# Kernel tuning notes

Hardware: AMD Instinct MI355X
Metric: run time of the kernel (lower is better)

The kernel has to match this reference:

```python
import jax, jax.numpy as jnp
import numpy as np

L = 3          # encoder layers
H, D = 12, 64  # heads, head_dim
DM = H * D     # 768
DF = 3072
WH = WW = 14
S = WH * WW + 1            # 197 tokens incl. cls
ND = (2*WH-1)*(2*WW-1) + 3  # 732 rel-pos entries
EPS = 1e-12


def _make_rel_idx():
    coords = np.stack(np.meshgrid(np.arange(WH), np.arange(WW), indexing='ij'))
    coords = coords.reshape(2, -1)                      # [2, 196]
    rel = (coords[:, :, None] - coords[:, None, :]).transpose(1, 2, 0)  # [196,196,2]
    rel[:, :, 0] += WH - 1
    rel[:, :, 1] += WW - 1
    rel[:, :, 0] *= 2 * WW - 1
    idx = np.zeros((S, S), dtype=np.int32)
    idx[1:, 1:] = rel.sum(-1)
    idx[0, :] = ND - 3
    idx[:, 0] = ND - 2
    idx[0, 0] = ND - 1
    return jnp.asarray(idx.flatten())

REL_IDX = _make_rel_idx()


def _ln(x, g, b):
    m = jnp.mean(x, -1, keepdims=True)
    v = jnp.mean(jnp.square(x - m), -1, keepdims=True)
    return (x - m) * jax.lax.rsqrt(v + EPS) * g + b


def setup_inputs() -> dict:
    key = jax.random.key(0)
    ks = iter(jax.random.split(key, 32))
    p = lambda *s: jax.random.normal(next(ks), s, jnp.float32) * 0.02
    inp = {
        'x': jax.random.normal(next(ks), (64, WH, WW, DM), jnp.float32),
        'cls': p(1, 1, DM),
        'g1': jnp.ones((L, DM)), 'b1': jnp.zeros((L, DM)),
        'Wq': p(L, DM, DM), 'bq': jnp.zeros((L, DM)),
        'Wk': p(L, DM, DM),
        'Wv': p(L, DM, DM), 'bv': jnp.zeros((L, DM)),
        'rel_tbl': p(L, ND, H),
        'Wo': p(L, DM, DM), 'bo': jnp.zeros((L, DM)),
        'lam1': jnp.full((L, DM), 0.1),
        'g2': jnp.ones((L, DM)), 'b2': jnp.zeros((L, DM)),
        'Wi': p(L, DM, DF), 'bi': jnp.zeros((L, DF)),
        'Wmo': p(L, DF, DM), 'bmo': jnp.zeros((L, DM)),
        'lam2': jnp.full((L, DM), 0.1),
    }
    return inp


def reference(x, cls, g1, b1, Wq, bq, Wk, Wv, bv, rel_tbl, Wo, bo, lam1,
              g2, b2, Wi, bi, Wmo, bmo, lam2):
    B = x.shape[0]
    # patchemb: NHWC -> NCHW -> [B, C, HW] -> [B, HW, C], prepend cls token
    t = jnp.transpose(x, (0, 3, 1, 2)).reshape(B, DM, WH * WW)
    t = jnp.transpose(t, (0, 2, 1))
    h = jnp.concatenate([jnp.broadcast_to(cls, (B, 1, DM)), t], axis=1)  # [B,S,DM]

    scale = 1.0 / np.sqrt(D)
    for i in range(L):
        r = h
        hn = _ln(h, g1[i], b1[i])
        q = (hn @ Wq[i] + bq[i]).reshape(B, S, H, D)
        k = (hn @ Wk[i]).reshape(B, S, H, D)
        v = (hn @ Wv[i] + bv[i]).reshape(B, S, H, D)
        scores = jnp.einsum('bqhd,bkhd->bhqk', q, k) * scale   # [B,H,S,S]
        rel = rel_tbl[i][REL_IDX].reshape(S, S, H)             # gather bias table
        scores = scores + jnp.transpose(rel, (2, 0, 1))[None]
        probs = jax.nn.softmax(scores, axis=-1)
        ctx = jnp.einsum('bhqk,bkhd->bqhd', probs, v).reshape(B, S, DM)
        h = r + (ctx @ Wo[i] + bo[i]) * lam1[i]
        r = h
        hn = _ln(h, g2[i], b2[i])
        ff = jax.nn.gelu(hn @ Wi[i] + bi[i], approximate=False) @ Wmo[i] + bmo[i]
        h = r + ff * lam2[i]
    return h  # final encoder output [B, S, DM]
```

## Files before the change

### kernel.cpp

```cpp
#include <hip/hip_runtime.h>

#define DMM 768
#define DFF 3072
#define NH  12
#define HD  64
#define SQ  197
#define BA  64
#define NDD 732
#define MROWS (BA*SQ)
#define MPAD  12672
#define PCOLS 224
#define KS2   72
#define VTS   232
#define QS    2304
#define BIASN (NH*208*208)

typedef unsigned short u16;
typedef __bf16 bf16x8 __attribute__((ext_vector_type(8)));
typedef float  f32x4  __attribute__((ext_vector_type(4)));
typedef unsigned short us8 __attribute__((ext_vector_type(8)));

__device__ __forceinline__ float b2f(u16 u) {
    unsigned v = ((unsigned)u) << 16;
    float f; __builtin_memcpy(&f, &v, 4); return f;
}
__device__ __forceinline__ u16 f2b(float f) {
    unsigned v; __builtin_memcpy(&v, &f, 4);
    unsigned r = v + 0x7FFFu + ((v >> 16) & 1u);
    return (u16)(r >> 16);
}
__device__ __forceinline__ float gelu_exact(float x) {
    return 0.5f * x * (1.0f + erff(x * 0.70710678118654752f));
}
__device__ __forceinline__ void gload16(const u16* g, u16* l) {
    __builtin_amdgcn_global_load_lds(
        (const __attribute__((address_space(1))) unsigned int*)(g),
        (__attribute__((address_space(3))) unsigned int*)(l), 16, 0, 0);
}
__device__ __forceinline__ void hard_barrier() {
    asm volatile("s_waitcnt lgkmcnt(0)" ::: "memory");
    __builtin_amdgcn_s_barrier();
}

__global__ void patch_k(const float* __restrict__ x, const float* __restrict__ cls,
                        float* __restrict__ h) {
    long idx = (long)blockIdx.x * 256 + threadIdx.x;
    if (idx >= (long)MPAD * DMM) return;
    long r = idx / DMM; int c = (int)(idx % DMM);
    float v = 0.0f;
    if (r < MROWS) {
        int b = (int)(r / SQ), s = (int)(r % SQ);
        v = (s == 0) ? cls[c] : x[((long)b * 196 + (s - 1)) * DMM + c];
    }
    h[idx] = v;
}

__global__ void out_k(const float* __restrict__ h, float* __restrict__ out) {
    long idx = (long)blockIdx.x * 256 + threadIdx.x;
    if (idx < (long)MROWS * DMM) out[idx] = h[idx];
}

__global__ __launch_bounds__(256) void tcast_k(const float* __restrict__ in,
                                               u16* __restrict__ out,
                                               int Kd, int Nd) {
    __shared__ float t[32][33];
    int k0 = blockIdx.x * 32, n0 = blockIdx.y * 32;
    int tx = threadIdx.x & 31, ty = threadIdx.x >> 5;
    #pragma unroll
    for (int i = 0; i < 4; ++i)
        t[tx][ty + 8 * i] = in[(long)(k0 + ty + 8 * i) * Nd + n0 + tx];
    __syncthreads();
    #pragma unroll
    for (int i = 0; i < 4; ++i)
        out[(long)(n0 + ty + 8 * i) * Kd + k0 + tx] = f2b(t[ty + 8 * i][tx]);
}

__global__ __launch_bounds__(256) void tcast4_k(
    const float* __restrict__ s0, const float* __restrict__ s1,
    const float* __restrict__ s2, const float* __restrict__ s3,
    u16* __restrict__ d0, u16* __restrict__ d1,
    u16* __restrict__ d2, u16* __restrict__ d3) {
    __shared__ float t[32][33];
    int z = blockIdx.z;
    const float* in = (z == 0) ? s0 : (z == 1) ? s1 : (z == 2) ? s2 : s3;
    u16* out = (z == 0) ? d0 : (z == 1) ? d1 : (z == 2) ? d2 : d3;
    int k0 = blockIdx.x * 32, n0 = blockIdx.y * 32;
    int tx = threadIdx.x & 31, ty = threadIdx.x >> 5;
    #pragma unroll
    for (int i = 0; i < 4; ++i)
        t[tx][ty + 8 * i] = in[(long)(k0 + ty + 8 * i) * DMM + n0 + tx];
    __syncthreads();
    #pragma unroll
    for (int i = 0; i < 4; ++i)
        out[(long)(n0 + ty + 8 * i) * DMM + k0 + tx] = f2b(t[ty + 8 * i][tx]);
}

__global__ __launch_bounds__(256) void ln_k(const float* __restrict__ h,
                                            const float* __restrict__ g,
                                            const float* __restrict__ b,
                                            u16* __restrict__ hn) {
    int row = blockIdx.x, tid = threadIdx.x;
    const float* hr = h + (long)row * DMM;
    float x0 = hr[tid], x1 = hr[tid + 256], x2 = hr[tid + 512];
    float s = x0 + x1 + x2, sq = x0 * x0 + x1 * x1 + x2 * x2;
    #pragma unroll
    for (int m = 32; m > 0; m >>= 1) {
        s  += __shfl_xor(s,  m, 64);
        sq += __shfl_xor(sq, m, 64);
    }
    __shared__ float ls[4], lq[4];
    int w = tid >> 6;
    if ((tid & 63) == 0) { ls[w] = s; lq[w] = sq; }
    __syncthreads();
    s  = ls[0] + ls[1] + ls[2] + ls[3];
    sq = lq[0] + lq[1] + lq[2] + lq[3];
    float mean = s * (1.0f / DMM);
    float var  = fmaxf(sq * (1.0f / DMM) - mean * mean, 0.0f);
    float rs = rsqrtf(var + 1e-12f);
    u16* hnr = hn + (long)row * DMM;
    hnr[tid]       = f2b((x0 - mean) * rs * g[tid]       + b[tid]);
    hnr[tid + 256] = f2b((x1 - mean) * rs * g[tid + 256] + b[tid + 256]);
    hnr[tid + 512] = f2b((x2 - mean) * rs * g[tid + 512] + b[tid + 512]);
}

template <int EPI>
__global__ __launch_bounds__(256) void gemm_bt(
    const u16* __restrict__ A, const u16* __restrict__ BT,
    const float* __restrict__ bias, u16* __restrict__ outB,
    float* __restrict__ hio, const float* __restrict__ lam,
    int K, int N) {
    __shared__ __align__(16) u16 pool[24576];
    int tid = threadIdx.x;
    int w = tid >> 6, lane = tid & 63;
    int wr = w >> 1, wc = w & 1;
    int m16 = lane & 15;
    int kq  = (lane >> 4) * 8;
    int kq4 = (lane >> 4) * 4;

    int nwg = gridDim.x, bid = blockIdx.x;
    int qd = nwg >> 3, rm = nwg & 7;
    int xcd = bid & 7, seq = bid >> 3;
    int wg = (xcd < rm ? xcd * (qd + 1) : rm * (qd + 1) + (xcd - rm) * qd) + seq;
    int ntn = N >> 7;
    long m0 = (long)(wg / ntn) * 128;
    long n0 = (long)(wg % ntn) * 128;

    f32x4 acc[4][4] = {};

    int row_a = tid >> 2;
    int col_a = (tid & 3) * 8;
    const u16* gA0 = &A[(m0 + row_a) * (long)K + col_a];
    const u16* gA1 = &A[(m0 + 64 + row_a) * (long)K + col_a];
    const u16* gB0 = &BT[(n0 + row_a) * (long)K + col_a];
    const u16* gB1 = &BT[(n0 + 64 + row_a) * (long)K + col_a];
    int wo = w * 512;

    u16* const b0 = pool;
    u16* const b1 = pool + 8192;
    u16* const b2 = pool + 16384;

    auto stage = [&](int k, u16* buf) {
        int k0 = k << 5;
        gload16(gA0 + k0, buf + wo);
        gload16(gA1 + k0, buf + 2048 + wo);
        gload16(gB0 + k0, buf + 4096 + wo);
        gload16(gB1 + k0, buf + 6144 + wo);
    };
    auto compute = [&](const u16* buf) {
        bf16x8 af[4], bf[4];
        #pragma unroll
        for (int i = 0; i < 4; ++i)
            af[i] = *(const bf16x8*)&buf[(wr * 64 + i * 16 + m16) * 32 + kq];
        #pragma unroll
        for (int j = 0; j < 4; ++j)
            bf[j] = *(const bf16x8*)&buf[4096 + (wc * 64 + j * 16 + m16) * 32 + kq];
        __builtin_amdgcn_s_setprio(1);
        #pragma unroll
        for (int i = 0; i < 4; ++i)
            #pragma unroll
            for (int j = 0; j < 4; ++j)
                acc[i][j] = __builtin_amdgcn_mfma_f32_16x16x32_bf16(
                    af[i], bf[j], acc[i][j], 0, 0, 0);
        __builtin_amdgcn_s_setprio(0);
    };

    const int nsteps = K >> 5;
    stage(0, b0);
    stage(1, b1);
    const int niter = nsteps / 3 - 1;
    for (int it = 0; it < niter; ++it) {
        int k = it * 3;
        asm volatile("s_waitcnt vmcnt(4)" ::: "memory");
        __builtin_amdgcn_s_barrier();
        stage(k + 2, b2);
        compute(b0);
        asm volatile("s_waitcnt vmcnt(4)" ::: "memory");
        __builtin_amdgcn_s_barrier();
        stage(k + 3, b0);
        compute(b1);
        asm volatile("s_waitcnt vmcnt(4)" ::: "memory");
        __builtin_amdgcn_s_barrier();
        stage(k + 4, b1);
        compute(b2);
    }
    asm volatile("s_waitcnt vmcnt(4)" ::: "memory");
    __builtin_amdgcn_s_barrier();
    stage(nsteps - 1, b2);
    compute(b0);
    asm volatile("s_waitcnt vmcnt(4)" ::: "memory");
    __builtin_amdgcn_s_barrier();
    compute(b1);
    asm volatile("s_waitcnt vmcnt(0)" ::: "memory");
    __builtin_amdgcn_s_barrier();
    compute(b2);

    hard_barrier();
    float* Cs = (float*)pool;
    float bcol[4];
    #pragma unroll
    for (int j = 0; j < 4; ++j)
        bcol[j] = bias ? bias[n0 + wc * 64 + j * 16 + m16] : 0.0f;
    int et4 = tid * 4;
    int colr = et4 & 127;
    f32x4 lam4 = {};
    if (EPI == 2) lam4 = *(const f32x4*)&lam[n0 + colr];

    #pragma unroll
    for (int p = 0; p < 2; ++p) {
        if (p) hard_barrier();
        if (wr == p) {
            #pragma unroll
            for (int i = 0; i < 4; ++i)
                #pragma unroll
                for (int j = 0; j < 4; ++j)
                    #pragma unroll
                    for (int r = 0; r < 4; ++r)
                        Cs[(i * 16 + kq4 + r) * 132 + wc * 64 + j * 16 + m16] =
                            acc[i][j][r] + bcol[j];
        }
        hard_barrier();
        #pragma unroll
        for (int k = 0; k < 8; ++k) {
            int e0 = k * 1024 + et4;
            int row = e0 >> 7;
            f32x4 v = *(const f32x4*)&Cs[row * 132 + colr];
            long gi = (m0 + p * 64 + row) * (long)N + n0 + colr;
            if (EPI == 0) {
                uint2 o;
                o.x = (unsigned)f2b(v[0]) | ((unsigned)f2b(v[1]) << 16);
                o.y = (unsigned)f2b(v[2]) | ((unsigned)f2b(v[3]) << 16);
                *(uint2*)&outB[gi] = o;
            } else if (EPI == 1) {
                uint2 o;
                o.x = (unsigned)f2b(gelu_exact(v[0])) | ((unsigned)f2b(gelu_exact(v[1])) << 16);
                o.y = (unsigned)f2b(gelu_exact(v[2])) | ((unsigned)f2b(gelu_exact(v[3])) << 16);
                *(uint2*)&outB[gi] = o;
            } else {
                f32x4 hv = *(f32x4*)&hio[gi];
                #pragma unroll
                for (int t = 0; t < 4; ++t) hv[t] += v[t] * lam4[t];
                *(f32x4*)&hio[gi] = hv;
            }
        }
    }
}

__device__ __forceinline__ int relidx(int q, int k) {
    if (q == 0 && k == 0) return NDD - 1;
    if (k == 0) return NDD - 2;
    if (q == 0) return NDD - 3;
    int a = q - 1, c = k - 1;
    int dh = a / 14 - c / 14 + 13;
    int dw = a % 14 - c % 14 + 13;
    return dh * 27 + dw;
}

__global__ void bias_k(const float* __restrict__ rel, float* __restrict__ bias,
                       const float* __restrict__ bq, const float* __restrict__ bv,
                       float* __restrict__ bqkv) {
    int idx = blockIdx.x * 256 + threadIdx.x;
    if (idx < BIASN) {
        int hh = idx / (208 * 208);
        int r = (idx / 208) % 208, c = idx % 208;
        float v = 0.0f;
        if (r < SQ && c < SQ) v = rel[relidx(r, c) * NH + hh];
        bias[idx] = v;
    } else {
        int i = idx - BIASN;
        if (i < QS)
            bqkv[i] = (i < 768) ? bq[i] : ((i < 1536) ? 0.0f : bv[i - 1536]);
    }
}

__global__ __launch_bounds__(256) void attn_qk(
    const u16* __restrict__ QKV, const float* __restrict__ bias,
    u16* __restrict__ P) {
    int bh = blockIdx.x;
    int b = bh / NH, hh = bh % NH;
    __shared__ u16 Ks[208 * KS2];
    int tid = threadIdx.x, w = tid >> 6, lane = tid & 63;
    long base = ((long)b * SQ) * QS + hh * HD;
    const u16* Qp = QKV;
    const u16* Kp = QKV + 768;
    u16* Pb = P + (long)bh * 208 * PCOLS;
    for (int idx = tid; idx < 208 * 16; idx += 256)
        Pb[(idx >> 4) * PCOLS + 208 + (idx & 15)] = 0;
    for (int idx = tid; idx < 208 * 8; idx += 256) {
        int row = idx >> 3, dg = (idx & 7) * 8;
        us8 kv = {};
        if (row < SQ) kv = *(const us8*)&Kp[base + (long)row * QS + dg];
        *(us8*)&Ks[row * KS2 + dg] = kv;
    }
    __syncthreads();
    int m16 = lane & 15, quad = lane >> 4;
    int kq8 = quad * 8, q4 = quad * 4;
    const float* bh_bias = bias + (long)hh * 208 * 208;
    for (int t = w; t < 13; t += 4) {
        int m0 = t * 16;
        int qrow = m0 + m16; if (qrow > SQ - 1) qrow = SQ - 1;
        bf16x8 a0 = *(const bf16x8*)&Qp[base + (long)qrow * QS + kq8];
        bf16x8 a1 = *(const bf16x8*)&Qp[base + (long)qrow * QS + 32 + kq8];
        f32x4 sc[13];
        #pragma unroll
        for (int n = 0; n < 13; ++n) {
            bf16x8 b0 = *(const bf16x8*)&Ks[(n * 16 + m16) * KS2 + kq8];
            bf16x8 b1 = *(const bf16x8*)&Ks[(n * 16 + m16) * KS2 + 32 + kq8];
            f32x4 z = {};
            z = __builtin_amdgcn_mfma_f32_16x16x32_bf16(a0, b0, z, 0, 0, 0);
            z = __builtin_amdgcn_mfma_f32_16x16x32_bf16(a1, b1, z, 0, 0, 0);
            sc[n] = z;
        }
        float mx[4] = {-3e38f, -3e38f, -3e38f, -3e38f};
        #pragma unroll
        for (int n = 0; n < 13; ++n) {
            int col = n * 16 + m16;
            bool valid = col < SQ;
            #pragma unroll
            for (int r = 0; r < 4; ++r) {
                float v = sc[n][r] * 0.125f + bh_bias[(m0 + q4 + r) * 208 + col];
                v = valid ? v : -3e38f;
                sc[n][r] = v;
                mx[r] = fmaxf(mx[r], v);
            }
        }
        #pragma unroll
        for (int r = 0; r < 4; ++r)
            #pragma unroll
            for (int msk = 1; msk < 16; msk <<= 1)
                mx[r] = fmaxf(mx[r], __shfl_xor(mx[r], msk, 64));
        float sum[4] = {0, 0, 0, 0};
        #pragma unroll
        for (int n = 0; n < 13; ++n)
            #pragma unroll
            for (int r = 0; r < 4; ++r) {
                float e = __expf(sc[n][r] - mx[r]);
                sc[n][r] = e;
                sum[r] += e;
            }
        #pragma unroll
        for (int r = 0; r < 4; ++r)
            #pragma unroll
            for (int msk = 1; msk < 16; msk <<= 1)
                sum[r] += __shfl_xor(sum[r], msk, 64);
        float inv[4];
        #pragma unroll
        for (int r = 0; r < 4; ++r) inv[r] = 1.0f / sum[r];
        #pragma unroll
        for (int n = 0; n < 13; ++n) {
            int col = n * 16 + m16;
            #pragma unroll
            for (int r = 0; r < 4; ++r)
                Pb[(m0 + q4 + r) * PCOLS + col] = f2b(sc[n][r] * inv[r]);
        }
    }
}

__global__ __launch_bounds__(256) void attn_pv(
    const u16* __restrict__ P, const u16* __restrict__ QKV,
    u16* __restrict__ ctx) {
    int bh = blockIdx.x;
    int b = bh / NH, hh = bh % NH;
    __shared__ u16 Vt[64 * VTS];
    int tid = threadIdx.x, w = tid >> 6, lane = tid & 63;
    long base  = ((long)b * SQ) * QS + 1536 + hh * HD;
    long basec = ((long)b * SQ) * DMM + hh * HD;
    const u16* Vp = QKV;
    for (int idx = tid; idx < 224 * 8; idx += 256) {
        int row = idx >> 3, dg = (idx & 7) * 8;
        us8 vv = {};
        if (row < SQ) vv = *(const us8*)&Vp[base + (long)row * QS + dg];
        #pragma unroll
        for (int j = 0; j < 8; ++j) Vt[(dg + j) * VTS + row] = vv[j];
    }
    __syncthreads();
    const u16* Pb = P + (long)bh * 208 * PCOLS;
    int m16 = lane & 15, quad = lane >> 4;
    int kq8 = quad * 8, q4 = quad * 4;
    for (int t = w; t < 13; t += 4) {
        int m0 = t * 16;
        f32x4 co[4] = {};
        #pragma unroll
        for (int ks = 0; ks < 7; ++ks) {
            bf16x8 ap = *(const bf16x8*)&Pb[(m0 + m16) * PCOLS + ks * 32 + kq8];
            #pragma unroll
            for (int n = 0; n < 4; ++n) {
                bf16x8 bv = *(const bf16x8*)&Vt[(n * 16 + m16) * VTS + ks * 32 + kq8];
                co[n] = __builtin_amdgcn_mfma_f32_16x16x32_bf16(ap, bv, co[n], 0, 0, 0);
            }
        }
        #pragma unroll
        for (int n = 0; n < 4; ++n) {
            int col = n * 16 + m16;
            #pragma unroll
            for (int r = 0; r < 4; ++r) {
                int qr = m0 + q4 + r;
                if (qr < SQ) ctx[basec + (long)qr * DMM + col] = f2b(co[n][r]);
            }
        }
    }
}

extern "C" void kernel_launch(void* const* d_in, const int* in_sizes, int n_in,
                              void* d_out, int out_size, void* d_ws, size_t ws_size,
                              hipStream_t stream) {
    const float* x    = (const float*)d_in[0];
    const float* cls  = (const float*)d_in[1];
    const float* g1   = (const float*)d_in[2];
    const float* b1   = (const float*)d_in[3];
    const float* Wq   = (const float*)d_in[4];
    const float* bq   = (const float*)d_in[5];
    const float* Wk   = (const float*)d_in[6];
    const float* Wv   = (const float*)d_in[7];
    const float* bv   = (const float*)d_in[8];
    const float* rel  = (const float*)d_in[9];
    const float* Wo   = (const float*)d_in[10];
    const float* bo   = (const float*)d_in[11];
    const float* lam1 = (const float*)d_in[12];
    const float* g2   = (const float*)d_in[13];
    const float* b2   = (const float*)d_in[14];
    const float* Wi   = (const float*)d_in[15];
    const float* bi   = (const float*)d_in[16];
    const float* Wmo  = (const float*)d_in[17];
    const float* bmo  = (const float*)d_in[18];
    const float* lam2 = (const float*)d_in[19];

    char* p = (char*)d_ws;
    auto alloc = [&](size_t bytes) -> void* {
        void* r = (void*)p;
        p += (bytes + 255) & ~(size_t)255;
        return r;
    };
    float* h     = (float*)alloc((size_t)MPAD * DMM * 4);
    u16*   hn    = (u16*)alloc((size_t)MPAD * DMM * 2);
    u16*   qkvb  = (u16*)alloc((size_t)MPAD * QS * 2);
    u16*   ffh   = (u16*)alloc((size_t)MPAD * DFF * 2);
    u16*   WqkvT = (u16*)alloc((size_t)QS * DMM * 2);
    u16*   WoT   = (u16*)alloc((size_t)DMM * DMM * 2);
    u16*   WiT   = (u16*)alloc((size_t)DMM * DFF * 2);
    u16*   WmoT  = (u16*)alloc((size_t)DFF * DMM * 2);
    float* biasb = (float*)alloc((size_t)NH * 208 * 208 * 4);
    float* bqkv  = (float*)alloc((size_t)QS * 4);
    u16*   ctxb  = hn;
    u16*   Pbuf  = ffh;

    patch_k<<<((long)MPAD * DMM + 255) / 256, 256, 0, stream>>>(x, cls, h);

    dim3 tg4(DMM / 32, DMM / 32, 4);
    dim3 tg2(DMM / 32, DFF / 32);
    dim3 tg3(DFF / 32, DMM / 32);
    int gqkv = (MPAD / 128) * (QS / 128);
    int g6   = (MPAD / 128) * (DMM / 128);
    int g24  = (MPAD / 128) * (DFF / 128);

    for (int i = 0; i < 3; ++i) {
        size_t wofs  = (size_t)i * DMM * DMM;
        size_t wofs2 = (size_t)i * DMM * DFF;
        tcast4_k<<<tg4, 256, 0, stream>>>(Wq + wofs, Wk + wofs, Wv + wofs, Wo + wofs,
                                          WqkvT, WqkvT + 768 * DMM,
                                          WqkvT + 2 * 768 * DMM, WoT);
        tcast_k<<<tg2, 256, 0, stream>>>(Wi + wofs2, WiT, DMM, DFF);
        tcast_k<<<tg3, 256, 0, stream>>>(Wmo + wofs2, WmoT, DFF, DMM);
        bias_k<<<(BIASN + QS + 255) / 256, 256, 0, stream>>>(
            rel + (size_t)i * NDD * NH, biasb, bq + i * DMM, bv + i * DMM, bqkv);

        ln_k<<<MPAD, 256, 0, stream>>>(h, g1 + i * DMM, b1 + i * DMM, hn);
        gemm_bt<0><<<gqkv, 256, 0, stream>>>(hn, WqkvT, bqkv, qkvb, nullptr, nullptr, DMM, QS);
        attn_qk<<<BA * NH, 256, 0, stream>>>(qkvb, biasb, Pbuf);
        attn_pv<<<BA * NH, 256, 0, stream>>>(Pbuf, qkvb, ctxb);
        gemm_bt<2><<<g6, 256, 0, stream>>>(ctxb, WoT, bo + i * DMM, nullptr, h, lam1 + i * DMM, DMM, DMM);
        ln_k<<<MPAD, 256, 0, stream>>>(h, g2 + i * DMM, b2 + i * DMM, hn);
        gemm_bt<1><<<g24, 256, 0, stream>>>(hn, WiT, bi + i * DFF, ffh, nullptr, nullptr, DMM, DFF);
        gemm_bt<2><<<g6, 256, 0, stream>>>(ffh, WmoT, bmo + i * DMM, nullptr, h, lam2 + i * DMM, DFF, DMM);
    }

    out_k<<<((long)MROWS * DMM + 255) / 256, 256, 0, stream>>>(h, (float*)d_out);
}
```

Measured before the change: 1.378 ms.

## Replace 128x128 GEMM with 256x256-tile 8-wave kernel using swizzled LDS

Replaces the 128x128, 4-wave triple-buffered GEMM with a 256x256-tile, 512-thread kernel. It uses 128KB of dynamic LDS with XOR-swizzled layout, K-step 64, double buffering and a four-phase schedule that interleaves global loads with MFMA. Bias is now added in the epilogue, and MPAD is raised to a multiple of 256. The goal is more operand reuse per tile and fewer LDS bank conflicts, at the cost of fewer workgroups: the DMM-width GEMMs get only 150 tiles on 256 CUs. The new kernel also carries a larger register footprint.

```diff
diff --git a/kernel.cpp b/kernel.cpp
--- a/kernel.cpp
+++ b/kernel.cpp
@@ -8,7 +8,7 @@
 #define BA  64
 #define NDD 732
 #define MROWS (BA*SQ)
-#define MPAD  12672
+#define MPAD  12800
 #define PCOLS 224
 #define KS2   72
 #define VTS   232
@@ -124,145 +124,158 @@
 }
 
 template <int EPI>
-__global__ __launch_bounds__(256) void gemm_bt(
+__global__ __launch_bounds__(512) void gemm256(
     const u16* __restrict__ A, const u16* __restrict__ BT,
     const float* __restrict__ bias, u16* __restrict__ outB,
     float* __restrict__ hio, const float* __restrict__ lam,
     int K, int N) {
-    __shared__ __align__(16) u16 pool[24576];
+    extern __shared__ __align__(16) u16 pool[];
     int tid = threadIdx.x;
     int w = tid >> 6, lane = tid & 63;
-    int wr = w >> 1, wc = w & 1;
+    int wm = w >> 2, wn = w & 3;
     int m16 = lane & 15;
-    int kq  = (lane >> 4) * 8;
-    int kq4 = (lane >> 4) * 4;
+    int q = lane >> 4, kq4 = q * 4;
+    int r7 = m16 & 7;
 
     int nwg = gridDim.x, bid = blockIdx.x;
     int qd = nwg >> 3, rm = nwg & 7;
     int xcd = bid & 7, seq = bid >> 3;
     int wg = (xcd < rm ? xcd * (qd + 1) : rm * (qd + 1) + (xcd - rm) * qd) + seq;
-    int ntn = N >> 7;
-    long m0 = (long)(wg / ntn) * 128;
-    long n0 = (long)(wg % ntn) * 128;
-
-    f32x4 acc[4][4] = {};
-
-    int row_a = tid >> 2;
-    int col_a = (tid & 3) * 8;
-    const u16* gA0 = &A[(m0 + row_a) * (long)K + col_a];
-    const u16* gA1 = &A[(m0 + 64 + row_a) * (long)K + col_a];
-    const u16* gB0 = &BT[(n0 + row_a) * (long)K + col_a];
-    const u16* gB1 = &BT[(n0 + 64 + row_a) * (long)K + col_a];
-    int wo = w * 512;
-
-    u16* const b0 = pool;
-    u16* const b1 = pool + 8192;
-    u16* const b2 = pool + 16384;
-
-    auto stage = [&](int k, u16* buf) {
-        int k0 = k << 5;
-        gload16(gA0 + k0, buf + wo);
-        gload16(gA1 + k0, buf + 2048 + wo);
-        gload16(gB0 + k0, buf + 4096 + wo);
-        gload16(gB1 + k0, buf + 6144 + wo);
-    };
-    auto compute = [&](const u16* buf) {
-        bf16x8 af[4], bf[4];
-        #pragma unroll
-        for (int i = 0; i < 4; ++i)
-            af[i] = *(const bf16x8*)&buf[(wr * 64 + i * 16 + m16) * 32 + kq];
-        #pragma unroll
-        for (int j = 0; j < 4; ++j)
-            bf[j] = *(const bf16x8*)&buf[4096 + (wc * 64 + j * 16 + m16) * 32 + kq];
-        __builtin_amdgcn_s_setprio(1);
-        #pragma unroll
-        for (int i = 0; i < 4; ++i)
-            #pragma unroll
-            for (int j = 0; j < 4; ++j)
-                acc[i][j] = __builtin_amdgcn_mfma_f32_16x16x32_bf16(
-                    af[i], bf[j], acc[i][j], 0, 0, 0);
-        __builtin_amdgcn_s_setprio(0);
-    };
-
-    const int nsteps = K >> 5;
-    stage(0, b0);
-    stage(1, b1);
-    const int niter = nsteps / 3 - 1;
-    for (int it = 0; it < niter; ++it) {
-        int k = it * 3;
-        asm volatile("s_waitcnt vmcnt(4)" ::: "memory");
-        __builtin_amdgcn_s_barrier();
-        stage(k + 2, b2);
-        compute(b0);
-        asm volatile("s_waitcnt vmcnt(4)" ::: "memory");
-        __builtin_amdgcn_s_barrier();
-        stage(k + 3, b0);
-        compute(b1);
-        asm volatile("s_waitcnt vmcnt(4)" ::: "memory");
-        __builtin_amdgcn_s_barrier();
-        stage(k + 4, b1);
-        compute(b2);
-    }
+    int ntn = N >> 8;
+    long m0 = (long)(wg / ntn) * 256;
+    long n0 = (long)(wg % ntn) * 256;
+
+    int aK0 = wm * 16384 + m16 * 128 + ((q ^ r7) << 4);
+    int aK1 = wm * 16384 + m16 * 128 + (((4 + q) ^ r7) << 4);
+    int bK0 = 65536 + (wn >> 1) * 16384 + (((wn & 1) * 64 + m16) << 7) + ((q ^ r7) << 4);
+    int bK1 = 65536 + (wn >> 1) * 16384 + (((wn & 1) * 64 + m16) << 7) + (((4 + q) ^ r7) << 4);
+
+    int lrow = (w << 3) | (lane >> 3);
+    int colsw = ((lane & 7) ^ (lane >> 3)) << 3;
+    const u16* gAr = A  + (m0 + lrow) * (long)K + colsw;
+    const u16* gBr = BT + (n0 + lrow) * (long)K + colsw;
+    u16* ldsA = pool + w * 512;
+    u16* ldsB = pool + 32768 + w * 512;
+
+#define STGA(d, h, kt) do {                                                 \
+    const u16* s_ = gAr + (h) * 128 * (long)K + (kt) * 64;                  \
+    gload16(s_,              ldsA + (d) * 16384 + (h) * 8192);              \
+    gload16(s_ + 64 * (long)K, ldsA + (d) * 16384 + (h) * 8192 + 4096);     \
+} while (0)
+#define STGB(d, h, kt) do {                                                 \
+    const u16* s_ = gBr + (h) * 128 * (long)K + (kt) * 64;                  \
+    gload16(s_,              ldsB + (d) * 16384 + (h) * 8192);              \
+    gload16(s_ + 64 * (long)K, ldsB + (d) * 16384 + (h) * 8192 + 4096);     \
+} while (0)
+#define RDA(d, fm, kk) (*(const bf16x8*)((const char*)pool + ((d) << 15) + aK##kk + (fm) * 2048))
+#define RDB(d, fn, kk) (*(const bf16x8*)((const char*)pool + ((d) << 15) + bK##kk + (fn) * 2048))
+
+    f32x4 acc[8][4] = {};
+    bf16x8 bf[4][2];
+
+#define PHASE(d, ph, DOA, ktA, DOB, ktB, VM) do {                           \
+    if ((ph) == 0) {                                                        \
+        _Pragma("unroll")                                                   \
+        for (int fn = 0; fn < 4; ++fn) {                                    \
+            bf[fn][0] = RDB(d, fn, 0);                                      \
+            bf[fn][1] = RDB(d, fn, 1);                                      \
+        }                                                                   \
+    }                                                                       \
+    bf16x8 a00 = RDA(d, 2 * (ph) + 0, 0), a01 = RDA(d, 2 * (ph) + 0, 1);    \
+    bf16x8 a10 = RDA(d, 2 * (ph) + 1, 0), a11 = RDA(d, 2 * (ph) + 1, 1);    \
+    if ((DOA) && (ph) == 0) STGA((d) ^ 1, 0, ktA);                          \
+    if ((DOA) && (ph) == 1) STGA((d) ^ 1, 1, ktA);                          \
+    if ((DOB) && (ph) == 2) STGB(d, 0, ktB);                                \
+    if ((DOB) && (ph) == 3) STGB(d, 1, ktB);                                \
+    __builtin_amdgcn_s_barrier();                                           \
+    asm volatile("s_waitcnt lgkmcnt(0)" ::: "memory");                      \
+    __builtin_amdgcn_sched_barrier(0);                                      \
+    __builtin_amdgcn_s_setprio(1);                                          \
+    _Pragma("unroll")                                                       \
+    for (int fn = 0; fn < 4; ++fn) {                                        \
+        acc[2*(ph)+0][fn] = __builtin_amdgcn_mfma_f32_16x16x32_bf16(a00, bf[fn][0], acc[2*(ph)+0][fn], 0, 0, 0); \
+        acc[2*(ph)+0][fn] = __builtin_amdgcn_mfma_f32_16x16x32_bf16(a01, bf[fn][1], acc[2*(ph)+0][fn], 0, 0, 0); \
+        acc[2*(ph)+1][fn] = __builtin_amdgcn_mfma_f32_16x16x32_bf16(a10, bf[fn][0], acc[2*(ph)+1][fn], 0, 0, 0); \
+        acc[2*(ph)+1][fn] = __builtin_amdgcn_mfma_f32_16x16x32_bf16(a11, bf[fn][1], acc[2*(ph)+1][fn], 0, 0, 0); \
+    }                                                                       \
+    __builtin_amdgcn_s_setprio(0);                                          \
+    if ((VM) == 4) asm volatile("s_waitcnt vmcnt(4)" ::: "memory");         \
+    if ((VM) == 0) asm volatile("s_waitcnt vmcnt(0)" ::: "memory");         \
+    __builtin_amdgcn_s_barrier();                                           \
+} while (0)
+
+#define WINDOW(d, ktA, DOA, ktB, DOB, VM)                                   \
+    PHASE(d, 0, DOA, ktA, 0, 0, -1);                                        \
+    PHASE(d, 1, DOA, ktA, 0, 0, -1);                                        \
+    PHASE(d, 2, 0, 0, DOB, ktB, -1);                                        \
+    PHASE(d, 3, 0, 0, DOB, ktB, VM);
+
+    STGA(0, 0, 0); STGA(0, 1, 0); STGB(0, 0, 0); STGB(0, 1, 0);
+    STGB(1, 0, 1); STGB(1, 1, 1);
     asm volatile("s_waitcnt vmcnt(4)" ::: "memory");
     __builtin_amdgcn_s_barrier();
-    stage(nsteps - 1, b2);
-    compute(b0);
-    asm volatile("s_waitcnt vmcnt(4)" ::: "memory");
-    __builtin_amdgcn_s_barrier();
-    compute(b1);
-    asm volatile("s_waitcnt vmcnt(0)" ::: "memory");
-    __builtin_amdgcn_s_barrier();
-    compute(b2);
-
-    hard_barrier();
+
+    const int nt = K >> 6;
+    for (int t = 0; t < nt - 2; t += 2) {
+        WINDOW(0, t + 1, 1, t + 2, 1, 4);
+        WINDOW(1, t + 2, 1, t + 3, 1, 4);
+    }
+    WINDOW(0, nt - 1, 1, 0, 0, 0);
+    WINDOW(1, 0, 0, 0, 0, -1);
+
     float* Cs = (float*)pool;
-    float bcol[4];
+    int colc = (tid & 63) * 4;
+    int rb = tid >> 6;
+    f32x4 bias4 = *(const f32x4*)&bias[n0 + colc];
+    f32x4 lam4 = {};
+    if (EPI == 2) lam4 = *(const f32x4*)&lam[n0 + colc];
+
     #pragma unroll
-    for (int j = 0; j < 4; ++j)
-        bcol[j] = bias ? bias[n0 + wc * 64 + j * 16 + m16] : 0.0f;
-    int et4 = tid * 4;
-    int colr = et4 & 127;
-    f32x4 lam4 = {};
-    if (EPI == 2) lam4 = *(const f32x4*)&lam[n0 + colr];
-
-    #pragma unroll
-    for (int p = 0; p < 2; ++p) {
-        if (p) hard_barrier();
-        if (wr == p) {
-            #pragma unroll
-            for (int i = 0; i < 4; ++i)
+    for (int p2 = 0; p2 < 2; ++p2) {
+        if (p2) hard_barrier();
+        if (wm == p2) {
+            #pragma unroll
+            for (int fm = 0; fm < 8; ++fm)
                 #pragma unroll
-                for (int j = 0; j < 4; ++j)
+                for (int fn = 0; fn < 4; ++fn)
                     #pragma unroll
-                    for (int r = 0; r < 4; ++r)
-                        Cs[(i * 16 + kq4 + r) * 132 + wc * 64 + j * 16 + m16] =
-                            acc[i][j][r] + bcol[j];
+                    for (int rr = 0; rr < 4; ++rr)
+                        Cs[(fm * 16 + kq4 + rr) * 256 + wn * 64 + fn * 16 + m16] =
+                            acc[fm][fn][rr];
         }
         hard_barrier();
         #pragma unroll
-        for (int k = 0; k < 8; ++k) {
-            int e0 = k * 1024 + et4;
-            int row = e0 >> 7;
-            f32x4 v = *(const f32x4*)&Cs[row * 132 + colr];
-            long gi = (m0 + p * 64 + row) * (long)N + n0 + colr;
+        for (int k = 0; k < 16; ++k) {
+            int row = rb + k * 8;
+            f32x4 v = *(const f32x4*)&Cs[row * 256 + colc];
+            long gi = (m0 + p2 * 128 + row) * (long)N + n0 + colc;
             if (EPI == 0) {
                 uint2 o;
-                o.x = (unsigned)f2b(v[0]) | ((unsigned)f2b(v[1]) << 16);
-                o.y = (unsigned)f2b(v[2]) | ((unsigned)f2b(v[3]) << 16);
+                o.x = (unsigned)f2b(v[0] + bias4[0]) | ((unsigned)f2b(v[1] + bias4[1]) << 16);
+                o.y = (unsigned)f2b(v[2] + bias4[2]) | ((unsigned)f2b(v[3] + bias4[3]) << 16);
                 *(uint2*)&outB[gi] = o;
             } else if (EPI == 1) {
                 uint2 o;
-                o.x = (unsigned)f2b(gelu_exact(v[0])) | ((unsigned)f2b(gelu_exact(v[1])) << 16);
-                o.y = (unsigned)f2b(gelu_exact(v[2])) | ((unsigned)f2b(gelu_exact(v[3])) << 16);
+                o.x = (unsigned)f2b(gelu_exact(v[0] + bias4[0])) |
+                      ((unsigned)f2b(gelu_exact(v[1] + bias4[1])) << 16);
+                o.y = (unsigned)f2b(gelu_exact(v[2] + bias4[2])) |
+                      ((unsigned)f2b(gelu_exact(v[3] + bias4[3])) << 16);
                 *(uint2*)&outB[gi] = o;
             } else {
                 f32x4 hv = *(f32x4*)&hio[gi];
                 #pragma unroll
-                for (int t = 0; t < 4; ++t) hv[t] += v[t] * lam4[t];
+                for (int t4 = 0; t4 < 4; ++t4)
+                    hv[t4] += (v[t4] + bias4[t4]) * lam4[t4];
                 *(f32x4*)&hio[gi] = hv;
             }
         }
     }
+#undef STGA
+#undef STGB
+#undef RDA
+#undef RDB
+#undef PHASE
+#undef WINDOW
 }
 
 __device__ __forceinline__ int relidx(int q, int k) {
@@ -468,9 +481,10 @@
     dim3 tg4(DMM / 32, DMM / 32, 4);
     dim3 tg2(DMM / 32, DFF / 32);
     dim3 tg3(DFF / 32, DMM / 32);
-    int gqkv = (MPAD / 128) * (QS / 128);
-    int g6   = (MPAD / 128) * (DMM / 128);
-    int g24  = (MPAD / 128) * (DFF / 128);
+    int gqkv = (MPAD / 256) * (QS / 256);
+    int g6   = (MPAD / 256) * (DMM / 256);
+    int g24  = (MPAD / 256) * (DFF / 256);
+    const size_t LDSB = 131072;
 
     for (int i = 0; i < 3; ++i) {
         size_t wofs  = (size_t)i * DMM * DMM;
@@ -484,13 +498,13 @@
             rel + (size_t)i * NDD * NH, biasb, bq + i * DMM, bv + i * DMM, bqkv);
 
         ln_k<<<MPAD, 256, 0, stream>>>(h, g1 + i * DMM, b1 + i * DMM, hn);
-        gemm_bt<0><<<gqkv, 256, 0, stream>>>(hn, WqkvT, bqkv, qkvb, nullptr, nullptr, DMM, QS);
+        gemm256<0><<<gqkv, 512, LDSB, stream>>>(hn, WqkvT, bqkv, qkvb, nullptr, nullptr, DMM, QS);
         attn_qk<<<BA * NH, 256, 0, stream>>>(qkvb, biasb, Pbuf);
         attn_pv<<<BA * NH, 256, 0, stream>>>(Pbuf, qkvb, ctxb);
-        gemm_bt<2><<<g6, 256, 0, stream>>>(ctxb, WoT, bo + i * DMM, nullptr, h, lam1 + i * DMM, DMM, DMM);
+        gemm256<2><<<g6, 512, LDSB, stream>>>(ctxb, WoT, bo + i * DMM, nullptr, h, lam1 + i * DMM, DMM, DMM);
         ln_k<<<MPAD, 256, 0, stream>>>(h, g2 + i * DMM, b2 + i * DMM, hn);
-        gemm_bt<1><<<g24, 256, 0, stream>>>(hn, WiT, bi + i * DFF, ffh, nullptr, nullptr, DMM, DFF);
-        gemm_bt<2><<<g6, 256, 0, stream>>>(ffh, WmoT, bmo + i * DMM, nullptr, h, lam2 + i * DMM, DFF, DMM);
+        gemm256<1><<<g24, 512, LDSB, stream>>>(hn, WiT, bi + i * DFF, ffh, nullptr, nullptr, DMM, DFF);
+        gemm256<2><<<g6, 512, LDSB, stream>>>(ffh, WmoT, bmo + i * DMM, nullptr, h, lam2 + i * DMM, DFF, DMM);
     }
 
     out_k<<<((long)MROWS * DMM + 255) / 256, 256, 0, stream>>>(h, (float*)d_out);
```

New measurement: 1.353 ms. About the same (-1.8%).
